# Kernel tuning notes

Measured on AMD Instinct MI355X. Metric: run time of the kernel, lower is better.

Reference implementation:

```python
import jax, jax.numpy as jnp
import numpy as np

K = 3  # kernel_size

def setup_inputs() -> dict:
    key = jax.random.key(0)
    k1, k2, k3 = jax.random.split(key, 3)
    B, C, H, W = 8, 64, 128, 128
    x = jax.random.normal(k1, (B, C, H, W), dtype=jnp.float32)
    # 1x1 conv weight (out_channels*K*K, in_channels) and bias
    W_gen = jax.random.normal(k2, (C * K * K, C), dtype=jnp.float32) / np.float32(np.sqrt(C))
    b_gen = jax.random.normal(k3, (C * K * K,), dtype=jnp.float32) * 0.01
    return {"x": x, "W_gen": W_gen, "b_gen": b_gen}

def reference(x, W_gen, b_gen):
    B, C, H, W = x.shape  # out_channels == in_channels (required by the view)
    # filter_gen: 1x1 conv + ReLU -> (B, C*K*K, H, W)
    f = jax.nn.relu(jnp.einsum('bchw,oc->bohw', x, W_gen) + b_gen[None, :, None, None])
    filters = f.reshape(B, C, K * K, H, W)
    # F.unfold with padding=(K-1)//2, stride 1: gather KxK patches per pixel.
    pad = (K - 1) // 2
    xp = jnp.pad(x, ((0, 0), (0, 0), (pad, pad), (pad, pad)))
    # kernel-position index runs row-major (i*K + j), matching unfold layout
    patches = jnp.stack([xp[:, :, i:i + H, j:j + W]
                         for i in range(K) for j in range(K)], axis=2)  # (B,C,K*K,H,W)
    out = (filters * patches).sum(axis=2)  # (B,C,H,W)
    return out
```

## Files before the change

kernel.cpp:

```cpp
#include <hip/hip_runtime.h>
#include <hip/hip_bf16.h>

#define CC 64
#define HH 128
#define WW 128
#define OO 576
#define HW (HH * WW)

typedef __attribute__((ext_vector_type(8))) short short8;
typedef __attribute__((ext_vector_type(4))) float floatx4;

__device__ __forceinline__ unsigned short f2bf(float f) {
    unsigned u = __float_as_uint(f);
    u = (u + 0x7FFFu + ((u >> 16) & 1u)) >> 16;
    return (unsigned short)u;
}

__global__ void ACDA_wconv_kernel(const float* __restrict__ Wg,
                                  unsigned short* __restrict__ Wb) {
    int i = blockIdx.x * 256 + threadIdx.x;
    if (i < OO * CC) Wb[i] = f2bf(Wg[i]);
}

__global__ __launch_bounds__(256) void ACDA_main_kernel(
    const float* __restrict__ x, const unsigned short* __restrict__ Wb,
    const float* __restrict__ bg, float* __restrict__ out)
{
    __shared__ float Fbuf[4][16][68];

    const int tid  = threadIdx.x;
    const int wv   = tid >> 6;
    const int lane = tid & 63;
    const int quad = lane >> 4;
    const int l16  = lane & 15;

    const int bid = blockIdx.x;
    const int b   = bid & 7;
    const int j   = bid >> 3;
    const int seg = j & 1;
    const int h   = (j >> 1) & 127;
    const int w0  = seg << 6;

    const float* xb = x + (size_t)b * CC * HW;

    short8 bfrag[4][2];
#pragma unroll
    for (int nt = 0; nt < 4; ++nt) {
#pragma unroll
        for (int ks = 0; ks < 2; ++ks) {
            short8 v;
            const int w = w0 + nt * 16 + l16;
#pragma unroll
            for (int jj = 0; jj < 8; jj += 2) {
                const int c = ks * 32 + quad * 8 + jj;
                float f0 = xb[(c * HH + h) * WW + w];
                float f1 = xb[((c + 1) * HH + h) * WW + w];
                __hip_bfloat162 p = __float22bfloat162_rn(make_float2(f0, f1));
                unsigned u;
                __builtin_memcpy(&u, &p, 4);
                v[jj]     = (short)(u & 0xffffu);
                v[jj + 1] = (short)(u >> 16);
            }
            bfrag[nt][ks] = v;
        }
    }

    int wA = w0 + lane - 1; bool badA = (wA < 0);   if (badA) wA = 0;
    int wB = w0 + lane;
    int wC = w0 + lane + 1; bool badC = (wC > 127); if (badC) wC = 127;
    int rt[3]; bool rbad[3];
#pragma unroll
    for (int di = 0; di < 3; ++di) {
        int rr = h + di - 1;
        rbad[di] = (rr < 0) || (rr > 127);
        rr = rr < 0 ? 0 : (rr > 127 ? 127 : rr);
        rt[di] = rr * WW;
    }
    const int wsel[3]  = {wA, wB, wC};
    const bool wbad[3] = {badA, false, badC};
    const int soffC = wv * 16 * HW;
    int  pb[3][3]; bool bad[3][3];
#pragma unroll
    for (int di = 0; di < 3; ++di)
#pragma unroll
        for (int dj = 0; dj < 3; ++dj) {
            pb[di][dj]  = soffC + rt[di] + wsel[dj];
            bad[di][dj] = rbad[di] || wbad[dj];
        }

    float oacc[16];
#pragma unroll
    for (int i = 0; i < 16; ++i) oacc[i] = 0.f;

#pragma unroll
    for (int t = 0; t < 9; ++t) {
        const int obase = wv * 144 + t * 16;
        const unsigned short* wrow = Wb + (obase + l16) * CC + quad * 8;
        short8 a0 = *(const short8*)(wrow);
        short8 a1 = *(const short8*)(wrow + 32);
        floatx4 acc[4];
#pragma unroll
        for (int nt = 0; nt < 4; ++nt) {
            floatx4 z = {0.f, 0.f, 0.f, 0.f};
            z = __builtin_amdgcn_mfma_f32_16x16x32_bf16(a0, bfrag[nt][0], z, 0, 0, 0);
            z = __builtin_amdgcn_mfma_f32_16x16x32_bf16(a1, bfrag[nt][1], z, 0, 0, 0);
            acc[nt] = z;
        }
#pragma unroll
        for (int nt = 0; nt < 4; ++nt)
#pragma unroll
            for (int reg = 0; reg < 4; ++reg)
                Fbuf[wv][quad * 4 + reg][nt * 16 + l16] = acc[nt][reg];

#pragma unroll
        for (int r = 0; r < 16; ++r) {
            const int idx   = t * 16 + r;
            const int c_rel = idx / 9;
            const int kk    = idx - 9 * c_rel;
            const int di    = kk / 3;
            const int dj    = kk - 3 * di;
            float fv = Fbuf[wv][r][lane] + bg[obase + r];
            fv = fmaxf(fv, 0.f);
            float pv = xb[pb[di][dj] + c_rel * HW];
            if (bad[di][dj]) pv = 0.f;
            oacc[c_rel] = fmaf(fv, pv, oacc[c_rel]);
        }
    }

    float* ob = out + (size_t)b * CC * HW + h * WW + w0 + lane;
#pragma unroll
    for (int i = 0; i < 16; ++i)
        ob[(wv * 16 + i) * HW] = oacc[i];
}

extern "C" void kernel_launch(void* const* d_in, const int* in_sizes, int n_in,
                              void* d_out, int out_size, void* d_ws, size_t ws_size,
                              hipStream_t stream) {
    const float* x  = (const float*)d_in[0];
    const float* Wg = (const float*)d_in[1];
    const float* bg = (const float*)d_in[2];
    float* out = (float*)d_out;
    unsigned short* Wb = (unsigned short*)d_ws;

    ACDA_wconv_kernel<<<dim3((OO * CC + 255) / 256), dim3(256), 0, stream>>>(Wg, Wb);
    ACDA_main_kernel<<<dim3(8 * 128 * 2), dim3(256), 0, stream>>>(x, Wb, bg, out);
}
```

Measured before the change: 121.6 us.

## Permute weights by tap so MFMA outputs feed the product directly, dropping the LDS staging

The prep kernel now reorders the generated-filter weights and bias so that each MFMA tile of 16 rows covers one tap t across 16 channels. The MFMA accumulator layout then lines up with the output channel and pixel mapping, so the shared-memory Fbuf round trip is removed and the bias is folded into the accumulator init. Taps whose row falls outside the image are skipped, and launch bounds ask for 4 blocks per SM. The cost is a scattered prep write and per-element gathers of x with a different access pattern.

```diff
diff --git a/kernel.cpp b/kernel.cpp
--- a/kernel.cpp
+++ b/kernel.cpp
@@ -16,18 +16,26 @@
     return (unsigned short)u;
 }
 
-__global__ void ACDA_wconv_kernel(const float* __restrict__ Wg,
-                                  unsigned short* __restrict__ Wb) {
+__global__ void ACDA_prep_kernel(const float* __restrict__ Wg,
+                                 const float* __restrict__ bg,
+                                 unsigned short* __restrict__ Wbp,
+                                 float* __restrict__ bgp) {
     int i = blockIdx.x * 256 + threadIdx.x;
-    if (i < OO * CC) Wb[i] = f2bf(Wg[i]);
+    if (i < OO * CC) {
+        int o = i >> 6, k = i & 63;
+        int c = o / 9, t = o - 9 * c;
+        Wbp[(t * 64 + c) * 64 + k] = f2bf(Wg[i]);
+    }
+    if (i < OO) {
+        int c = i / 9, t = i - 9 * c;
+        bgp[t * 64 + c] = bg[i];
+    }
 }
 
-__global__ __launch_bounds__(256) void ACDA_main_kernel(
-    const float* __restrict__ x, const unsigned short* __restrict__ Wb,
-    const float* __restrict__ bg, float* __restrict__ out)
+__global__ __launch_bounds__(256, 4) void ACDA_main_kernel(
+    const float* __restrict__ x, const unsigned short* __restrict__ Wbp,
+    const float* __restrict__ bgp, float* __restrict__ out)
 {
-    __shared__ float Fbuf[4][16][68];
-
     const int tid  = threadIdx.x;
     const int wv   = tid >> 6;
     const int lane = tid & 63;
@@ -41,7 +49,7 @@
     const int h   = (j >> 1) & 127;
     const int w0  = seg << 6;
 
-    const float* xb = x + (size_t)b * CC * HW;
+    const float* __restrict__ xb = x + (size_t)b * CC * HW;
 
     short8 bfrag[4][2];
 #pragma unroll
@@ -49,10 +57,10 @@
 #pragma unroll
         for (int ks = 0; ks < 2; ++ks) {
             short8 v;
-            const int w = w0 + nt * 16 + l16;
+            const unsigned w = (unsigned)(w0 + nt * 16 + l16);
 #pragma unroll
             for (int jj = 0; jj < 8; jj += 2) {
-                const int c = ks * 32 + quad * 8 + jj;
+                const unsigned c = (unsigned)(ks * 32 + quad * 8 + jj);
                 float f0 = xb[(c * HH + h) * WW + w];
                 float f1 = xb[((c + 1) * HH + h) * WW + w];
                 __hip_bfloat162 p = __float22bfloat162_rn(make_float2(f0, f1));
@@ -65,72 +73,69 @@
         }
     }
 
-    int wA = w0 + lane - 1; bool badA = (wA < 0);   if (badA) wA = 0;
-    int wB = w0 + lane;
-    int wC = w0 + lane + 1; bool badC = (wC > 127); if (badC) wC = 127;
-    int rt[3]; bool rbad[3];
+    unsigned colofs[3][4];
 #pragma unroll
-    for (int di = 0; di < 3; ++di) {
-        int rr = h + di - 1;
-        rbad[di] = (rr < 0) || (rr > 127);
-        rr = rr < 0 ? 0 : (rr > 127 ? 127 : rr);
-        rt[di] = rr * WW;
-    }
-    const int wsel[3]  = {wA, wB, wC};
-    const bool wbad[3] = {badA, false, badC};
-    const int soffC = wv * 16 * HW;
-    int  pb[3][3]; bool bad[3][3];
+    for (int dj = 0; dj < 3; ++dj)
 #pragma unroll
-    for (int di = 0; di < 3; ++di)
+        for (int nt = 0; nt < 4; ++nt) {
+            int col = w0 + nt * 16 + l16 + dj - 1;
+            col = col < 0 ? 0 : (col > 127 ? 127 : col);
+            colofs[dj][nt] = (unsigned)col;
+        }
+    const bool badL = (w0 == 0)  && (l16 == 0);
+    const bool badR = (w0 == 64) && (l16 == 15);
+
+    unsigned cbase[4];
 #pragma unroll
-        for (int dj = 0; dj < 3; ++dj) {
-            pb[di][dj]  = soffC + rt[di] + wsel[dj];
-            bad[di][dj] = rbad[di] || wbad[dj];
-        }
+    for (int reg = 0; reg < 4; ++reg)
+        cbase[reg] = (unsigned)((wv * 16 + quad * 4 + reg) * HW);
 
-    float oacc[16];
+    float oacc[4][4];
 #pragma unroll
-    for (int i = 0; i < 16; ++i) oacc[i] = 0.f;
+    for (int nt = 0; nt < 4; ++nt)
+#pragma unroll
+        for (int reg = 0; reg < 4; ++reg) oacc[nt][reg] = 0.f;
 
 #pragma unroll
     for (int t = 0; t < 9; ++t) {
-        const int obase = wv * 144 + t * 16;
-        const unsigned short* wrow = Wb + (obase + l16) * CC + quad * 8;
-        short8 a0 = *(const short8*)(wrow);
-        short8 a1 = *(const short8*)(wrow + 32);
-        floatx4 acc[4];
+        const int di  = t / 3;
+        const int dj  = t - 3 * di;
+        const int row = h + di - 1;
+        if (row >= 0 && row < HH) {
+            const unsigned short* wrow =
+                Wbp + ((t * 64 + wv * 16 + l16) * 64 + quad * 8);
+            short8 a0 = *(const short8*)(wrow);
+            short8 a1 = *(const short8*)(wrow + 32);
+            floatx4 bq = *(const floatx4*)(bgp + t * 64 + wv * 16 + quad * 4);
+            floatx4 acc[4];
 #pragma unroll
-        for (int nt = 0; nt < 4; ++nt) {
-            floatx4 z = {0.f, 0.f, 0.f, 0.f};
-            z = __builtin_amdgcn_mfma_f32_16x16x32_bf16(a0, bfrag[nt][0], z, 0, 0, 0);
-            z = __builtin_amdgcn_mfma_f32_16x16x32_bf16(a1, bfrag[nt][1], z, 0, 0, 0);
-            acc[nt] = z;
-        }
+            for (int nt = 0; nt < 4; ++nt) {
+                floatx4 z = bq;
+                z = __builtin_amdgcn_mfma_f32_16x16x32_bf16(a0, bfrag[nt][0], z, 0, 0, 0);
+                z = __builtin_amdgcn_mfma_f32_16x16x32_bf16(a1, bfrag[nt][1], z, 0, 0, 0);
+                acc[nt] = z;
+            }
+            const unsigned rp = (unsigned)(row * WW);
 #pragma unroll
-        for (int nt = 0; nt < 4; ++nt)
+            for (int nt = 0; nt < 4; ++nt)
 #pragma unroll
-            for (int reg = 0; reg < 4; ++reg)
-                Fbuf[wv][quad * 4 + reg][nt * 16 + l16] = acc[nt][reg];
-
-#pragma unroll
-        for (int r = 0; r < 16; ++r) {
-            const int idx   = t * 16 + r;
-            const int c_rel = idx / 9;
-            const int kk    = idx - 9 * c_rel;
-            const int di    = kk / 3;
-            const int dj    = kk - 3 * di;
-            float fv = Fbuf[wv][r][lane] + bg[obase + r];
-            fv = fmaxf(fv, 0.f);
-            float pv = xb[pb[di][dj] + c_rel * HW];
-            if (bad[di][dj]) pv = 0.f;
-            oacc[c_rel] = fmaf(fv, pv, oacc[c_rel]);
+                for (int reg = 0; reg < 4; ++reg) {
+                    unsigned idx = cbase[reg] + rp + colofs[dj][nt];
+                    float pv = xb[idx];
+                    if (dj == 0 && nt == 0) pv = badL ? 0.f : pv;
+                    if (dj == 2 && nt == 3) pv = badR ? 0.f : pv;
+                    float fv = fmaxf(acc[nt][reg], 0.f);
+                    oacc[nt][reg] = fmaf(fv, pv, oacc[nt][reg]);
+                }
         }
     }
 
-    float* ob = out + (size_t)b * CC * HW + h * WW + w0 + lane;
+    float* ob = out + (size_t)b * CC * HW + h * WW + w0;
 #pragma unroll
-    for (int i = 0; i < 16; ++i)
-        ob[(wv * 16 + i) * HW] = oacc[i];
+    for (int nt = 0; nt < 4; ++nt)
+#pragma unroll
+        for (int reg = 0; reg < 4; ++reg)
+            ob[(wv * 16 + quad * 4 + reg) * HW + nt * 16 + l16] = oacc[nt][reg];
 }
 
 extern "C" void kernel_launch(void* const* d_in, const int* in_sizes, int n_in,
@@ -140,8 +145,9 @@
     const float* Wg = (const float*)d_in[1];
     const float* bg = (const float*)d_in[2];
     float* out = (float*)d_out;
-    unsigned short* Wb = (unsigned short*)d_ws;
+    unsigned short* Wbp = (unsigned short*)d_ws;
+    float* bgp = (float*)((char*)d_ws + OO * CC * 2);
 
-    ACDA_wconv_kernel<<<dim3((OO * CC + 255) / 256), dim3(256), 0, stream>>>(Wg, Wb);
-    ACDA_main_kernel<<<dim3(8 * 128 * 2), dim3(256), 0, stream>>>(x, Wb, bg, out);
+    ACDA_prep_kernel<<<dim3((OO * CC + 255) / 256), dim3(256), 0, stream>>>(Wg, bg, Wbp, bgp);
+    ACDA_main_kernel<<<dim3(8 * 128 * 2), dim3(256), 0, stream>>>(x, Wbp, bgp, out);
 }
```

After: 136.7 us. 1.12x slower.
